# Performance work log

Measured on AMD Instinct MI355X. Metric: run time of the kernel, lower is better.

The kernel has to match this reference:

```python
import jax, jax.numpy as jnp
import numpy as np

N, E, L = 50000, 800000, 3
EPS = 1e-5


def mlp2(h, W1, b1, W2, b2):
    # Linear -> ReLU -> Linear
    return jax.nn.relu(h @ W1 + b1) @ W2 + b2


def setup_inputs() -> dict:
    key = jax.random.key(0)
    ks = jax.random.split(key, 20)
    s = 0.1  # weight scale to keep activations well-conditioned
    return {
        "x": jax.random.normal(ks[0], (N, 128), jnp.float32),
        "edge_attr": jax.random.normal(ks[1], (E, 64), jnp.float32),
        "edge_index": jax.random.randint(ks[2], (2, E), 0, N, dtype=jnp.int32),
        "Wn1": jax.random.normal(ks[3], (L, 128, 256), jnp.float32) * s,
        "bn1": jnp.zeros((L, 256), jnp.float32),
        "Wn2": jax.random.normal(ks[4], (L, 256, 128), jnp.float32) * s,
        "bn2": jnp.zeros((L, 128), jnp.float32),
        "We1": jax.random.normal(ks[5], (L, 64, 128), jnp.float32) * s,
        "be1": jnp.zeros((L, 128), jnp.float32),
        "We2": jax.random.normal(ks[6], (L, 128, 64), jnp.float32) * s,
        "be2": jnp.zeros((L, 64), jnp.float32),
        "Wm1": jax.random.normal(ks[7], (L, 320, 128), jnp.float32) * s,
        "bm1": jnp.zeros((L, 128), jnp.float32),
        "Wm2": jax.random.normal(ks[8], (L, 128, 128), jnp.float32) * s,
        "bm2": jnp.zeros((L, 128), jnp.float32),
        "lnw": jnp.ones((L, 128), jnp.float32),
        "lnb": jnp.zeros((L, 128), jnp.float32),
        "Wf": jax.random.normal(ks[9], (128, 64), jnp.float32) * s,
        "bf": jnp.zeros((64,), jnp.float32),
    }


def reference(x, edge_attr, edge_index, Wn1, bn1, Wn2, bn2, We1, be1, We2, be2,
              Wm1, bm1, Wm2, bm2, lnw, lnb, Wf, bf):
    src, dst = edge_index[0], edge_index[1]  # x_j = x[src], x_i = x[dst] (PyG source_to_target)
    deg = jax.ops.segment_sum(jnp.ones((E,), x.dtype), dst, num_segments=N)
    denom = jnp.maximum(deg, 1.0)[:, None]  # scatter-mean with clamp for isolated nodes
    for l in range(L):
        # mlp_node is the same function for x_i and x_j -> apply once per node, then gather
        xn = mlp2(x, Wn1[l], bn1[l], Wn2[l], bn2[l])        # [N, 128]
        e = mlp2(edge_attr, We1[l], be1[l], We2[l], be2[l])  # [E, 64]
        m = jnp.concatenate([xn[dst], xn[src], e], axis=-1)  # [E, 320] = [x_i, x_j, edge_attr]
        m = mlp2(m, Wm1[l], bm1[l], Wm2[l], bm2[l])          # [E, 128]
        agg = jax.ops.segment_sum(m, dst, num_segments=N) / denom  # mean aggregate [N, 128]
        mu = agg.mean(-1, keepdims=True)
        var = agg.var(-1, keepdims=True)
        h = (agg - mu) * jax.lax.rsqrt(var + EPS) * lnw[l] + lnb[l]  # LayerNorm
        x = jax.nn.relu(h)  # dropout p=0.0 -> identity
    return x @ Wf + bf  # jk='last' -> final linear on last layer output
```

## Files before the change

### kernel.cpp

```cpp
#include <hip/hip_runtime.h>
#include <stdint.h>

#define NN 50000
#define NE 800000
#define NB 196

typedef float f32x4 __attribute__((ext_vector_type(4)));
typedef short bf16x8 __attribute__((ext_vector_type(8)));

__device__ __forceinline__ unsigned short f2bf(float f) {
  union { float f; unsigned u; } v; v.f = f;
  unsigned r = v.u + 0x7fffu + ((v.u >> 16) & 1u);
  return (unsigned short)(r >> 16);
}
__device__ __forceinline__ float bf2f(unsigned short h) {
  union { unsigned u; float f; } v; v.u = ((unsigned)h) << 16;
  return v.f;
}
__device__ __forceinline__ float ldf(const void* p, size_t i, int m32) {
  return m32 ? ((const float*)p)[i] : bf2f(((const unsigned short*)p)[i]);
}

__global__ void detect_kernel(const void* lnw, int* flag) {
  if (threadIdx.x == 0 && blockIdx.x == 0)
    *flag = (((const unsigned short*)lnw)[0] == 0x3F80) ? 0 : 1;
}

#define oWn1 0
#define oWn2 98304
#define oWm1 196608
#define oWe1 319488
#define oWe2 344064
#define oWm2 368640
#define oWf  417792
#define NWTOT 425984
#define obn1 0
#define obn2 768
#define obe1 1152
#define obe2 1536
#define obm1 1728
#define obm2 2112
#define olnw 2496
#define olnb 2880
#define obf  3264
#define NBTOT 3328

__global__ __launch_bounds__(256) void conv_w(
    const void* Wn1, const void* Wn2, const void* Wm1, const void* We1,
    const void* We2, const void* Wm2, const void* Wf,
    const int* __restrict__ flg, unsigned short* __restrict__ cW)
{
  const int m32 = *flg;
  int i = blockIdx.x * 256 + threadIdx.x;
  if (i >= NWTOT) return;
  const void* src; size_t j;
  if      (i < oWn2) { src = Wn1; j = i - oWn1; }
  else if (i < oWm1) { src = Wn2; j = i - oWn2; }
  else if (i < oWe1) { src = Wm1; j = i - oWm1; }
  else if (i < oWe2) { src = We1; j = i - oWe1; }
  else if (i < oWm2) { src = We2; j = i - oWe2; }
  else if (i < oWf)  { src = Wm2; j = i - oWm2; }
  else               { src = Wf;  j = i - oWf;  }
  cW[i] = f2bf(ldf(src, j, m32));
}

__global__ __launch_bounds__(256) void conv_b(
    const void* bn1, const void* bn2, const void* be1, const void* be2,
    const void* bm1, const void* bm2, const void* lnw, const void* lnb,
    const void* bfv, const int* __restrict__ flg, float* __restrict__ cB)
{
  const int m32 = *flg;
  int i = blockIdx.x * 256 + threadIdx.x;
  if (i >= NBTOT) return;
  const void* src; size_t j;
  if      (i < obn2) { src = bn1; j = i - obn1; }
  else if (i < obe1) { src = bn2; j = i - obn2; }
  else if (i < obe2) { src = be1; j = i - obe1; }
  else if (i < obm1) { src = be2; j = i - obe2; }
  else if (i < obm2) { src = bm1; j = i - obm1; }
  else if (i < olnw) { src = bm2; j = i - obm2; }
  else if (i < olnb) { src = lnw; j = i - olnw; }
  else if (i < obf)  { src = lnb; j = i - olnb; }
  else               { src = bfv; j = i - obf;  }
  cB[i] = ldf(src, j, m32);
}

__global__ __launch_bounds__(256) void conv_x(const void* x, const int* flg,
                                              unsigned short* xc) {
  const int m32 = *flg;
  size_t i = (size_t)blockIdx.x * 256 + threadIdx.x;
  if (i < (size_t)NN * 128) xc[i] = f2bf(ldf(x, i, m32));
}

__global__ __launch_bounds__(256) void deg_int(const int* __restrict__ eidx,
                                               int* __restrict__ degi) {
  int i = blockIdx.x * 256 + threadIdx.x;
  if (i < NE) atomicAdd(degi + eidx[NE + i], 1);
}

__global__ __launch_bounds__(256) void scan1(const int* __restrict__ degi,
                                             int* __restrict__ base,
                                             int* __restrict__ bsum) {
  __shared__ int s[256];
  int t = threadIdx.x, i = blockIdx.x * 256 + t;
  int v = (i < NN) ? degi[i] : 0;
  s[t] = v; __syncthreads();
  for (int d = 1; d < 256; d <<= 1) {
    int u = (t >= d) ? s[t - d] : 0;
    __syncthreads();
    s[t] += u;
    __syncthreads();
  }
  if (i < NN) base[i] = s[t] - v;
  if (t == 255) bsum[blockIdx.x] = s[255];
}

__global__ void scan2(int* bsum) {
  __shared__ int s[256];
  int t = threadIdx.x;
  int v = (t < NB) ? bsum[t] : 0;
  s[t] = v; __syncthreads();
  for (int d = 1; d < 256; d <<= 1) {
    int u = (t >= d) ? s[t - d] : 0;
    __syncthreads();
    s[t] += u;
    __syncthreads();
  }
  if (t < NB) bsum[t] = s[t] - v;
}

__global__ __launch_bounds__(256) void scan3(int* base, const int* bsum) {
  int i = blockIdx.x * 256 + threadIdx.x;
  if (i < NN) base[i] += bsum[blockIdx.x];
}

__global__ __launch_bounds__(256) void scatter_sort(
    const int* __restrict__ eidx, const int* __restrict__ base,
    int* __restrict__ cursor, int* __restrict__ sE,
    int* __restrict__ sSrc, int* __restrict__ sDst) {
  int e = blockIdx.x * 256 + threadIdx.x;
  if (e < NE) {
    int s = eidx[e], d = eidx[NE + e];
    int r = atomicAdd(cursor + d, 1);
    int pos = base[d] + r;
    sE[pos] = e; sSrc[pos] = s; sDst[pos] = d;
  }
}

__global__ __launch_bounds__(256) void gather_ea(
    const void* __restrict__ ea, const int* __restrict__ sE,
    const int* __restrict__ flg, unsigned short* __restrict__ eaS) {
  const int m32 = *flg;
  int slot = blockIdx.x * 32 + (threadIdx.x >> 3);
  int j = threadIdx.x & 7;
  if (slot >= NE) return;
  int eid = sE[slot];
  unsigned short* dst = eaS + (size_t)slot * 64 + j * 8;
  if (m32) {
    const float* src = (const float*)ea + (size_t)eid * 64 + j * 8;
    f32x4 v0 = *(const f32x4*)src;
    f32x4 v1 = *(const f32x4*)(src + 4);
    alignas(16) unsigned short t[8];
    #pragma unroll
    for (int q = 0; q < 4; q++) { t[q] = f2bf(v0[q]); t[4 + q] = f2bf(v1[q]); }
    *(bf16x8*)dst = *(const bf16x8*)t;
  } else {
    const unsigned short* src = (const unsigned short*)ea + (size_t)eid * 64 + j * 8;
    *(bf16x8*)dst = *(const bf16x8*)src;
  }
}

__global__ __launch_bounds__(256) void prep_wc(
    const unsigned short* __restrict__ cW, const float* __restrict__ cB,
    float* __restrict__ Wc, float* __restrict__ bc2)
{
  int l = blockIdx.x;
  const unsigned short* We2l = cW + oWe2 + l * 8192;
  const unsigned short* Wm1c = cW + oWm1 + l * 40960 + 256 * 128;
  const float* be2l = cB + obe2 + l * 64;
  const float* bm1l = cB + obm1 + l * 128;
  float* out = Wc + l * 16384;
  for (int i = threadIdx.x; i < 16384; i += 256) {
    int k = i >> 7, n = i & 127;
    float s = 0.f;
    for (int u = 0; u < 64; u++)
      s += bf2f(We2l[k * 64 + u]) * bf2f(Wm1c[u * 128 + n]);
    out[i] = s;
  }
  if (threadIdx.x < 128) {
    int n = threadIdx.x;
    float s = bm1l[n];
    for (int u = 0; u < 64; u++)
      s += bf2f(be2l[u]) * bf2f(Wm1c[u * 128 + n]);
    bc2[l * 128 + n] = s;
  }
}

__global__ __launch_bounds__(256) void pack_frags(
    const unsigned short* __restrict__ cW, const float* __restrict__ Wcp,
    unsigned short* __restrict__ Wn1p, unsigned short* __restrict__ Wn2p,
    unsigned short* __restrict__ Wm1p, unsigned short* __restrict__ We1p,
    unsigned short* __restrict__ Wcpk, unsigned short* __restrict__ Wm2p)
{
  int l = blockIdx.x / 6, which = blockIdx.x % 6;
  int K, N, total;
  const unsigned short* src = nullptr;
  const float* srcf = nullptr;
  unsigned short* dst;
  if (which == 0)      { K = 128; N = 256; src = cW + oWn1 + (size_t)l * 32768; dst = Wn1p + (size_t)l * 32768; }
  else if (which == 1) { K = 256; N = 128; src = cW + oWn2 + (size_t)l * 32768; dst = Wn2p + (size_t)l * 32768; }
  else if (which == 2) { K = 128; N = 256; src = cW + oWm1 + (size_t)l * 40960; dst = Wm1p + (size_t)l * 32768; }
  else if (which == 3) { K = 64;  N = 128; src = cW + oWe1 + (size_t)l * 8192;  dst = We1p + (size_t)l * 8192; }
  else if (which == 4) { K = 128; N = 128; srcf = Wcp + (size_t)l * 16384;      dst = Wcpk + (size_t)l * 16384; }
  else                 { K = 128; N = 128; src = cW + oWm2 + (size_t)l * 16384; dst = Wm2p + (size_t)l * 16384; }
  int KB = K >> 5;
  total = K * N;
  for (int o = threadIdx.x; o < total; o += 256) {
    int j = o & 7, lane = (o >> 3) & 63, q = o >> 9;
    int kb = q % KB, c = q / KB;
    int k = kb * 32 + (lane >> 4) * 8 + j;
    int n = c * 16 + (lane & 15);
    unsigned short v;
    if (which == 2) {
      v = (n < 128) ? src[k * 128 + n] : src[(128 + k) * 128 + (n - 128)];
    } else if (which == 4) {
      v = f2bf(srcf[k * 128 + n]);
    } else {
      v = src[k * N + n];
    }
    dst[o] = v;
  }
}

__global__ __launch_bounds__(256) void node_p_mfma(
    const unsigned short* __restrict__ xin,
    const unsigned short* __restrict__ Wn1p, const unsigned short* __restrict__ Wn2p,
    const unsigned short* __restrict__ Wm1p, const float* __restrict__ cB,
    unsigned short* __restrict__ P, int l)
{
  __shared__ __align__(16) short HS[4][16 * 256];
  const int tid = threadIdx.x;
  const int wid = tid >> 6, lane = tid & 63, rl = lane & 15, cg = lane >> 4;
  const int n0 = blockIdx.x * 64;
  short* Hw = &HS[wid][0];
  const int swr = (rl & 7) << 3;

  int nA = n0 + wid * 16 + rl;
  int nAc = (nA < NN) ? nA : (NN - 1);

  bf16x8 ax[4];
  {
    const unsigned short* xr = xin + (size_t)nAc * 128;
    #pragma unroll
    for (int kb = 0; kb < 4; kb++)
      ax[kb] = *(const bf16x8*)&xr[kb * 32 + cg * 8];
  }

  {
    const unsigned short* Wb = Wn1p + (size_t)l * 32768;
    const float* b1 = cB + obn1 + l * 256;
    #pragma unroll
    for (int c = 0; c < 16; c++) {
      f32x4 acc = {0.f, 0.f, 0.f, 0.f};
      #pragma unroll
      for (int kb = 0; kb < 4; kb++) {
        bf16x8 b = *(const bf16x8*)&Wb[(size_t)(c * 4 + kb) * 512 + lane * 8];
        acc = __builtin_amdgcn_mfma_f32_16x16x32_bf16(ax[kb], b, acc, 0, 0, 0);
      }
      int col = c * 16 + rl;
      float bb = b1[col];
      #pragma unroll
      for (int r = 0; r < 4; r++) {
        int row = cg * 4 + r;
        Hw[row * 256 + (col ^ ((row & 7) << 3))] =
            (short)f2bf(fmaxf(acc[r] + bb, 0.f));
      }
    }
  }

  {
    bf16x8 ah[8];
    #pragma unroll
    for (int kb = 0; kb < 8; kb++)
      ah[kb] = *(const bf16x8*)&Hw[rl * 256 + ((kb * 32 + cg * 8) ^ swr)];
    const unsigned short* Wb = Wn2p + (size_t)l * 32768;
    const float* b2 = cB + obn2 + l * 128;
    #pragma unroll
    for (int c = 0; c < 8; c++) {
      f32x4 acc = {0.f, 0.f, 0.f, 0.f};
      #pragma unroll
      for (int kb = 0; kb < 8; kb++) {
        bf16x8 b = *(const bf16x8*)&Wb[(size_t)(c * 8 + kb) * 512 + lane * 8];
        acc = __builtin_amdgcn_mfma_f32_16x16x32_bf16(ah[kb], b, acc, 0, 0, 0);
      }
      int col = c * 16 + rl;
      float bb = b2[col];
      #pragma unroll
      for (int r = 0; r < 4; r++) {
        int row = cg * 4 + r;
        Hw[row * 128 + (col ^ ((row & 7) << 3))] = (short)f2bf(acc[r] + bb);
      }
    }
  }

  {
    bf16x8 an[4];
    #pragma unroll
    for (int kb = 0; kb < 4; kb++)
      an[kb] = *(const bf16x8*)&Hw[rl * 128 + ((kb * 32 + cg * 8) ^ swr)];
    const unsigned short* Wb = Wm1p + (size_t)l * 32768;
    #pragma unroll
    for (int c = 0; c < 16; c++) {
      f32x4 acc = {0.f, 0.f, 0.f, 0.f};
      #pragma unroll
      for (int kb = 0; kb < 4; kb++) {
        bf16x8 b = *(const bf16x8*)&Wb[(size_t)(c * 4 + kb) * 512 + lane * 8];
        acc = __builtin_amdgcn_mfma_f32_16x16x32_bf16(an[kb], b, acc, 0, 0, 0);
      }
      int col = c * 16 + rl;
      #pragma unroll
      for (int r = 0; r < 4; r++) {
        int row = cg * 4 + r;
        Hw[row * 256 + (col ^ ((row & 7) << 3))] = (short)f2bf(acc[r]);
      }
    }
  }
  {
    int row = lane >> 2;
    int ch = (lane & 3) * 64;
    int n = n0 + wid * 16 + row;
    if (n < NN) {
      int sw = (row & 7) << 3;
      unsigned short* dst = P + (size_t)n * 256 + ch;
      #pragma unroll
      for (int g = 0; g < 8; g++) {
        bf16x8 v = *(const bf16x8*)&Hw[row * 256 + ((ch + g * 8) ^ sw)];
        *(bf16x8*)(dst + g * 8) = v;
      }
    }
  }
}

__global__ __launch_bounds__(256, 8) void edge_fold_v5(
    const unsigned short* __restrict__ eaS,
    const int* __restrict__ sSrc, const int* __restrict__ sDst,
    const int* __restrict__ baseg, const int* __restrict__ degg,
    const unsigned short* __restrict__ We1p, const unsigned short* __restrict__ Wcpk,
    const float* __restrict__ cB, const float* __restrict__ bc2,
    const unsigned short* __restrict__ P, float* __restrict__ agg, int l)
{
  __shared__ __align__(16) short hS[64 * 136];
  __shared__ int dstS[64], srcS[64];
  const int tid = threadIdx.x;
  const int wid = tid >> 6, lane = tid & 63, rl = lane & 15, cg = lane >> 4;
  const int e0 = blockIdx.x * 64;
  short* Rw = hS + wid * 2048;
  const int swr = (rl & 7) << 3;
  const int brow = wid * 16 + rl;

  if (cg == 0) {
    dstS[brow] = sDst[e0 + brow];
    srcS[brow] = sSrc[e0 + brow];
  }

  const unsigned short* er = eaS + (size_t)(e0 + brow) * 64;
  bf16x8 a0 = *(const bf16x8*)&er[cg * 8];
  bf16x8 a1 = *(const bf16x8*)&er[32 + cg * 8];

  {
    const unsigned short* Wb = We1p + (size_t)l * 8192;
    const float* be1l = cB + obe1 + l * 128;
    #pragma unroll
    for (int c = 0; c < 8; c++) {
      bf16x8 b0 = *(const bf16x8*)&Wb[(c * 2 + 0) * 512 + lane * 8];
      bf16x8 b1 = *(const bf16x8*)&Wb[(c * 2 + 1) * 512 + lane * 8];
      f32x4 acc = {0.f, 0.f, 0.f, 0.f};
      acc = __builtin_amdgcn_mfma_f32_16x16x32_bf16(a0, b0, acc, 0, 0, 0);
      acc = __builtin_amdgcn_mfma_f32_16x16x32_bf16(a1, b1, acc, 0, 0, 0);
      int col = c * 16 + rl;
      float b = be1l[col];
      #pragma unroll
      for (int r = 0; r < 4; r++) {
        int row = cg * 4 + r;
        Rw[row * 128 + (col ^ ((row & 7) << 3))] =
            (short)f2bf(fmaxf(acc[r] + b, 0.f));
      }
    }
  }

  f32x4 acc2[8];
  {
    bf16x8 ra[4];
    #pragma unroll
    for (int kb = 0; kb < 4; kb++)
      ra[kb] = *(const bf16x8*)&Rw[rl * 128 + ((kb * 32 + cg * 8) ^ swr)];
    const unsigned short* Wb = Wcpk + (size_t)l * 16384;
    #pragma unroll
    for (int c = 0; c < 8; c++) {
      f32x4 acc = {0.f, 0.f, 0.f, 0.f};
      #pragma unroll
      for (int kb = 0; kb < 4; kb++) {
        bf16x8 b = *(const bf16x8*)&Wb[(c * 4 + kb) * 512 + lane * 8];
        acc = __builtin_amdgcn_mfma_f32_16x16x32_bf16(ra[kb], b, acc, 0, 0, 0);
      }
      acc2[c] = acc;
    }
  }

  __syncthreads();

  {
    const float* bc2l = bc2 + l * 128;
    #pragma unroll
    for (int c = 0; c < 8; c++) {
      int col = c * 16 + rl;
      float bv = bc2l[col];
      #pragma unroll
      for (int r = 0; r < 4; r++) {
        int row = wid * 16 + cg * 4 + r;
        hS[row * 136 + (col ^ ((row & 7) << 3))] =
            (short)f2bf(acc2[c][r] + bv);
      }
    }
  }
  __syncthreads();

  {
    int row = tid & 63;
    int ch = (tid >> 6) * 32;
    int di = dstS[row], si = srcS[row];
    int sw = (row & 7) << 3;
    const unsigned short* Pd = P + (size_t)di * 256 + ch;
    const unsigned short* Ps = P + (size_t)si * 256 + 128 + ch;
    #pragma unroll
    for (int g = 0; g < 4; g++) {
      bf16x8 pd = *(const bf16x8*)(Pd + g * 8);
      bf16x8 ps = *(const bf16x8*)(Ps + g * 8);
      short* hp = &hS[row * 136 + ((ch + g * 8) ^ sw)];
      bf16x8 hv = *(const bf16x8*)hp;
      alignas(16) unsigned short o[8];
      #pragma unroll
      for (int j = 0; j < 8; j++) {
        float h = bf2f((unsigned short)hv[j]) + bf2f((unsigned short)pd[j]) +
                  bf2f((unsigned short)ps[j]);
        o[j] = f2bf(fmaxf(h, 0.f));
      }
      *(bf16x8*)hp = *(const bf16x8*)o;
    }
  }
  __syncthreads();

  if (tid < 128) {
    const int col = tid;
    float run = 0.f;
    int cur = dstS[0];
    for (int i = 0; i < 64; i++) {
      int d = dstS[i];
      if (d != cur) {
        int b0 = baseg[cur], dg = degg[cur];
        if (b0 >= e0 && b0 + dg <= e0 + 64)
          agg[(size_t)cur * 128 + col] = run;
        else
          atomicAdd(agg + (size_t)cur * 128 + col, run);
        run = 0.f; cur = d;
      }
      run += bf2f((unsigned short)hS[i * 136 + (col ^ ((i & 7) << 3))]);
    }
    int b0 = baseg[cur], dg = degg[cur];
    if (b0 >= e0 && b0 + dg <= e0 + 64)
      agg[(size_t)cur * 128 + col] = run;
    else
      atomicAdd(agg + (size_t)cur * 128 + col, run);
  }
}

__global__ __launch_bounds__(256, 8) void agg_ln_mfma(
    const float* __restrict__ aggH, const int* __restrict__ degi,
    const unsigned short* __restrict__ Wm2p, const float* __restrict__ cB,
    unsigned short* __restrict__ xnext, int l)
{
  __shared__ __align__(16) short OS[4][16 * 136];
  const int tid = threadIdx.x;
  const int wid = tid >> 6, lane = tid & 63, rl = lane & 15, cg = lane >> 4;
  const int n0 = blockIdx.x * 64;
  short* Ow = &OS[wid][0];

  int nA = n0 + wid * 16 + rl;
  int nAc = (nA < NN) ? nA : (NN - 1);
  int dA = degi[nAc];
  float degf = (float)dA;
  float invd = 1.f / (float)(dA > 0 ? dA : 1);

  bf16x8 af[4];
  {
    const float* ar = aggH + (size_t)nAc * 128;
    #pragma unroll
    for (int kb = 0; kb < 4; kb++) {
      f32x4 v0 = *(const f32x4*)&ar[kb * 32 + cg * 8];
      f32x4 v1 = *(const f32x4*)&ar[kb * 32 + cg * 8 + 4];
      alignas(16) unsigned short t[8];
      #pragma unroll
      for (int q = 0; q < 4; q++) {
        t[q] = f2bf(v0[q] * invd);
        t[4 + q] = f2bf(v1[q] * invd);
      }
      af[kb] = *(const bf16x8*)t;
    }
  }

  f32x4 acc[8];
  {
    const unsigned short* Wb = Wm2p + (size_t)l * 16384;
    #pragma unroll
    for (int c = 0; c < 8; c++) {
      f32x4 a = {0.f, 0.f, 0.f, 0.f};
      #pragma unroll
      for (int kb = 0; kb < 4; kb++) {
        bf16x8 b = *(const bf16x8*)&Wb[(c * 4 + kb) * 512 + lane * 8];
        a = __builtin_amdgcn_mfma_f32_16x16x32_bf16(af[kb], b, a, 0, 0, 0);
      }
      acc[c] = a;
    }
  }

  const float* bm2p = cB + obm2 + l * 128;
  const float* lnwp = cB + olnw + l * 128;
  const float* lnbp = cB + olnb + l * 128;
  #pragma unroll
  for (int r = 0; r < 4; r++) {
    int row = cg * 4 + r;
    float dg = __shfl(degf, row, 64);
    float bmask = (dg > 0.f) ? 1.f : 0.f;
    float v[8];
    float s = 0.f, q = 0.f;
    #pragma unroll
    for (int c = 0; c < 8; c++) {
      float x = acc[c][r] + bmask * bm2p[c * 16 + rl];
      v[c] = x; s += x; q += x * x;
    }
    #pragma unroll
    for (int m = 1; m < 16; m <<= 1) {
      s += __shfl_xor(s, m, 64);
      q += __shfl_xor(q, m, 64);
    }
    float mu = s * (1.f / 128.f);
    float var = fmaxf(q * (1.f / 128.f) - mu * mu, 0.f);
    float rs = rsqrtf(var + 1e-5f);
    #pragma unroll
    for (int c = 0; c < 8; c++) {
      int col = c * 16 + rl;
      float y = fmaxf((v[c] - mu) * rs * lnwp[col] + lnbp[col], 0.f);
      Ow[row * 136 + (col ^ ((row & 7) << 3))] = (short)f2bf(y);
    }
  }
  {
    int row = lane >> 2;
    int ch = (lane & 3) * 32;
    int n = n0 + wid * 16 + row;
    if (n < NN) {
      int sw = (row & 7) << 3;
      unsigned short* dst = xnext + (size_t)n * 128 + ch;
      #pragma unroll
      for (int g = 0; g < 4; g++) {
        bf16x8 v = *(const bf16x8*)&Ow[row * 136 + ((ch + g * 8) ^ sw)];
        *(bf16x8*)(dst + g * 8) = v;
      }
    }
  }
}

__global__ __launch_bounds__(256) void final_k(
    const unsigned short* __restrict__ xc, const unsigned short* __restrict__ cW,
    const float* __restrict__ cB, const int* __restrict__ flg,
    void* __restrict__ out)
{
  const int m32 = *flg;
  const int tid = threadIdx.x;
  const int t = tid & 63;
  const int nd = blockIdx.x * 4 + (tid >> 6);
  float acc = cB[obf + t];
  const unsigned short* xr = xc + (size_t)nd * 128;
  const unsigned short* W = cW + oWf + t;
  for (int k = 0; k < 128; k++)
    acc += bf2f(xr[k]) * bf2f(W[(size_t)k * 64]);
  if (m32) ((float*)out)[(size_t)nd * 64 + t] = acc;
  else ((unsigned short*)out)[(size_t)nd * 64 + t] = f2bf(acc);
}

extern "C" void kernel_launch(void* const* d_in, const int* in_sizes, int n_in,
                              void* d_out, int out_size, void* d_ws, size_t ws_size,
                              hipStream_t stream) {
  (void)in_sizes; (void)n_in; (void)out_size; (void)ws_size;
  const void* x    = d_in[0];
  const void* ea   = d_in[1];
  const int*  eidx = (const int*)d_in[2];
  const void* Wn1  = d_in[3];
  const void* bn1  = d_in[4];
  const void* Wn2  = d_in[5];
  const void* bn2  = d_in[6];
  const void* We1  = d_in[7];
  const void* be1  = d_in[8];
  const void* We2  = d_in[9];
  const void* be2  = d_in[10];
  const void* Wm1  = d_in[11];
  const void* bm1  = d_in[12];
  const void* Wm2  = d_in[13];
  const void* bm2  = d_in[14];
  const void* lnw  = d_in[15];
  const void* lnb  = d_in[16];
  const void* Wf   = d_in[17];
  const void* bfv  = d_in[18];

  char* ws = (char*)d_ws;
  size_t off = 0;
  auto alloc = [&](size_t bytes) {
    size_t o = off;
    off += (bytes + 255) & ~(size_t)255;
    return o;
  };
  int*            flag = (int*)(ws + alloc(4));
  unsigned short* xcur = (unsigned short*)(ws + alloc((size_t)NN * 128 * 2));
  unsigned short* Pb   = (unsigned short*)(ws + alloc((size_t)NN * 256 * 2));
  float*          aggH = (float*)(ws + alloc((size_t)NN * 128 * 4));
  unsigned short* cW   = (unsigned short*)(ws + alloc((size_t)NWTOT * 2));
  float*          cB   = (float*)(ws + alloc((size_t)NBTOT * 4));
  float*          Wcp  = (float*)(ws + alloc(3 * 16384 * 4));
  float*          bc2w = (float*)(ws + alloc(3 * 128 * 4));
  unsigned short* We1p = (unsigned short*)(ws + alloc(3 * 8192 * 2));
  unsigned short* Wcpk = (unsigned short*)(ws + alloc(3 * 16384 * 2));
  unsigned short* Wn1p = (unsigned short*)(ws + alloc(3 * 32768 * 2));
  unsigned short* Wn2p = (unsigned short*)(ws + alloc(3 * 32768 * 2));
  unsigned short* Wm1p = (unsigned short*)(ws + alloc(3 * 32768 * 2));
  unsigned short* Wm2p = (unsigned short*)(ws + alloc(3 * 16384 * 2));
  int*            degi = (int*)(ws + alloc((size_t)NN * 4));
  int*            baseb= (int*)(ws + alloc((size_t)NN * 4));
  int*            bsum = (int*)(ws + alloc(256 * 4));
  int*            curs = (int*)(ws + alloc((size_t)NN * 4));
  int*            sE   = (int*)(ws + alloc((size_t)NE * 4));
  int*            sSrc = (int*)(ws + alloc((size_t)NE * 4));
  int*            sDst = (int*)(ws + alloc((size_t)NE * 4));
  unsigned short* eaS  = (unsigned short*)(ws + alloc((size_t)NE * 64 * 2));

  detect_kernel<<<1, 64, 0, stream>>>(lnw, flag);
  conv_w<<<(NWTOT + 255) / 256, 256, 0, stream>>>(Wn1, Wn2, Wm1, We1, We2, Wm2,
                                                  Wf, flag, cW);
  conv_b<<<(NBTOT + 255) / 256, 256, 0, stream>>>(bn1, bn2, be1, be2, bm1, bm2,
                                                  lnw, lnb, bfv, flag, cB);
  conv_x<<<(NN * 128 + 255) / 256, 256, 0, stream>>>(x, flag, xcur);

  hipMemsetAsync(degi, 0, (size_t)NN * 4, stream);
  deg_int<<<(NE + 255) / 256, 256, 0, stream>>>(eidx, degi);
  scan1<<<NB, 256, 0, stream>>>(degi, baseb, bsum);
  scan2<<<1, 256, 0, stream>>>(bsum);
  scan3<<<NB, 256, 0, stream>>>(baseb, bsum);
  hipMemsetAsync(curs, 0, (size_t)NN * 4, stream);
  scatter_sort<<<(NE + 255) / 256, 256, 0, stream>>>(eidx, baseb, curs, sE,
                                                     sSrc, sDst);
  gather_ea<<<NE / 32, 256, 0, stream>>>(ea, sE, flag, eaS);

  prep_wc<<<3, 256, 0, stream>>>(cW, cB, Wcp, bc2w);
  pack_frags<<<18, 256, 0, stream>>>(cW, Wcp, Wn1p, Wn2p, Wm1p, We1p, Wcpk,
                                     Wm2p);

  for (int l = 0; l < 3; l++) {
    node_p_mfma<<<(NN + 63) / 64, 256, 0, stream>>>(xcur, Wn1p, Wn2p, Wm1p,
                                                    cB, Pb, l);
    hipMemsetAsync(aggH, 0, (size_t)NN * 128 * 4, stream);
    edge_fold_v5<<<NE / 64, 256, 0, stream>>>(eaS, sSrc, sDst, baseb, degi,
                                              We1p, Wcpk, cB, bc2w, Pb,
                                              aggH, l);
    agg_ln_mfma<<<(NN + 63) / 64, 256, 0, stream>>>(aggH, degi, Wm2p, cB,
                                                    xcur, l);
  }
  final_k<<<NN / 4, 256, 0, stream>>>(xcur, cW, cB, flag, d_out);
}
```

Measured before the change: 1.525 ms.

## Prefetch P gathers before barrier, split segment reduction across all threads, drop swizzle

The edge kernel now loads the src/dst indices straight into registers and issues the gathers of projected node features early, before the barrier that precedes the hS bias write. This lets gather latency overlap the MFMA epilogue. The segmented reduction now uses all 256 threads, with each half handling 32 edges, rather than only 128 threads walking 64. The XOR swizzle on the padded 136-stride LDS rows is removed in both edge_fold and agg_ln. Holding the prefetched data raises register pressure, so launch bounds go from 8 to 6 waves, and splitting the reduction produces more atomics at the half boundary.

```diff
diff --git a/kernel.cpp b/kernel.cpp
--- a/kernel.cpp
+++ b/kernel.cpp
@@ -341,7 +341,7 @@
   }
 }
 
-__global__ __launch_bounds__(256, 8) void edge_fold_v5(
+__global__ __launch_bounds__(256, 6) void edge_fold_v6(
     const unsigned short* __restrict__ eaS,
     const int* __restrict__ sSrc, const int* __restrict__ sDst,
     const int* __restrict__ baseg, const int* __restrict__ degg,
@@ -350,7 +350,7 @@
     const unsigned short* __restrict__ P, float* __restrict__ agg, int l)
 {
   __shared__ __align__(16) short hS[64 * 136];
-  __shared__ int dstS[64], srcS[64];
+  __shared__ int dstS[64];
   const int tid = threadIdx.x;
   const int wid = tid >> 6, lane = tid & 63, rl = lane & 15, cg = lane >> 4;
   const int e0 = blockIdx.x * 64;
@@ -358,10 +358,12 @@
   const int swr = (rl & 7) << 3;
   const int brow = wid * 16 + rl;
 
-  if (cg == 0) {
-    dstS[brow] = sDst[e0 + brow];
-    srcS[brow] = sSrc[e0 + brow];
-  }
+  if (cg == 0) dstS[brow] = sDst[e0 + brow];
+
+  const int row2 = tid & 63;
+  const int ch2 = (tid >> 6) * 32;
+  const int di2 = sDst[e0 + row2];
+  const int si2 = sSrc[e0 + row2];
 
   const unsigned short* er = eaS + (size_t)(e0 + brow) * 64;
   bf16x8 a0 = *(const bf16x8*)&er[cg * 8];
@@ -407,6 +409,17 @@
     }
   }
 
+  bf16x8 pd[4], ps[4];
+  {
+    const unsigned short* Pd = P + (size_t)di2 * 256 + ch2;
+    const unsigned short* Ps = P + (size_t)si2 * 256 + 128 + ch2;
+    #pragma unroll
+    for (int g = 0; g < 4; g++) {
+      pd[g] = *(const bf16x8*)(Pd + g * 8);
+      ps[g] = *(const bf16x8*)(Ps + g * 8);
+    }
+  }
+
   __syncthreads();
 
   {
@@ -418,31 +431,22 @@
       #pragma unroll
       for (int r = 0; r < 4; r++) {
         int row = wid * 16 + cg * 4 + r;
-        hS[row * 136 + (col ^ ((row & 7) << 3))] =
-            (short)f2bf(acc2[c][r] + bv);
+        hS[row * 136 + col] = (short)f2bf(acc2[c][r] + bv);
       }
     }
   }
   __syncthreads();
 
   {
-    int row = tid & 63;
-    int ch = (tid >> 6) * 32;
-    int di = dstS[row], si = srcS[row];
-    int sw = (row & 7) << 3;
-    const unsigned short* Pd = P + (size_t)di * 256 + ch;
-    const unsigned short* Ps = P + (size_t)si * 256 + 128 + ch;
     #pragma unroll
     for (int g = 0; g < 4; g++) {
-      bf16x8 pd = *(const bf16x8*)(Pd + g * 8);
-      bf16x8 ps = *(const bf16x8*)(Ps + g * 8);
-      short* hp = &hS[row * 136 + ((ch + g * 8) ^ sw)];
+      short* hp = &hS[row2 * 136 + ch2 + g * 8];
       bf16x8 hv = *(const bf16x8*)hp;
       alignas(16) unsigned short o[8];
       #pragma unroll
       for (int j = 0; j < 8; j++) {
-        float h = bf2f((unsigned short)hv[j]) + bf2f((unsigned short)pd[j]) +
-                  bf2f((unsigned short)ps[j]);
+        float h = bf2f((unsigned short)hv[j]) + bf2f((unsigned short)pd[g][j]) +
+                  bf2f((unsigned short)ps[g][j]);
         o[j] = f2bf(fmaxf(h, 0.f));
       }
       *(bf16x8*)hp = *(const bf16x8*)o;
@@ -450,24 +454,26 @@
   }
   __syncthreads();
 
-  if (tid < 128) {
-    const int col = tid;
+  {
+    const int col = tid & 127;
+    const int half = tid >> 7;
+    const int lo = half * 32, hi = lo + 32;
     float run = 0.f;
-    int cur = dstS[0];
-    for (int i = 0; i < 64; i++) {
+    int cur = dstS[lo];
+    for (int i = lo; i < hi; i++) {
       int d = dstS[i];
       if (d != cur) {
         int b0 = baseg[cur], dg = degg[cur];
-        if (b0 >= e0 && b0 + dg <= e0 + 64)
+        if (b0 >= e0 + lo && b0 + dg <= e0 + hi)
           agg[(size_t)cur * 128 + col] = run;
         else
           atomicAdd(agg + (size_t)cur * 128 + col, run);
         run = 0.f; cur = d;
       }
-      run += bf2f((unsigned short)hS[i * 136 + (col ^ ((i & 7) << 3))]);
+      run += bf2f((unsigned short)hS[i * 136 + col]);
     }
     int b0 = baseg[cur], dg = degg[cur];
-    if (b0 >= e0 && b0 + dg <= e0 + 64)
+    if (b0 >= e0 + lo && b0 + dg <= e0 + hi)
       agg[(size_t)cur * 128 + col] = run;
     else
       atomicAdd(agg + (size_t)cur * 128 + col, run);
@@ -550,7 +556,7 @@
     for (int c = 0; c < 8; c++) {
       int col = c * 16 + rl;
       float y = fmaxf((v[c] - mu) * rs * lnwp[col] + lnbp[col], 0.f);
-      Ow[row * 136 + (col ^ ((row & 7) << 3))] = (short)f2bf(y);
+      Ow[row * 136 + col] = (short)f2bf(y);
     }
   }
   {
@@ -558,11 +564,10 @@
     int ch = (lane & 3) * 32;
     int n = n0 + wid * 16 + row;
     if (n < NN) {
-      int sw = (row & 7) << 3;
       unsigned short* dst = xnext + (size_t)n * 128 + ch;
       #pragma unroll
       for (int g = 0; g < 4; g++) {
-        bf16x8 v = *(const bf16x8*)&Ow[row * 136 + ((ch + g * 8) ^ sw)];
+        bf16x8 v = *(const bf16x8*)&Ow[row * 136 + ch + g * 8];
         *(bf16x8*)(dst + g * 8) = v;
       }
     }
@@ -666,7 +671,7 @@
     node_p_mfma<<<(NN + 63) / 64, 256, 0, stream>>>(xcur, Wn1p, Wn2p, Wm1p,
                                                     cB, Pb, l);
     hipMemsetAsync(aggH, 0, (size_t)NN * 128 * 4, stream);
-    edge_fold_v5<<<NE / 64, 256, 0, stream>>>(eaS, sSrc, sDst, baseb, degi,
+    edge_fold_v6<<<NE / 64, 256, 0, stream>>>(eaS, sSrc, sDst, baseb, degi,
                                               We1p, Wcpk, cB, bc2w, Pb,
                                               aggH, l);
     agg_ln_mfma<<<(NN + 63) / 64, 256, 0, stream>>>(aggH, degi, Wm2p, cB,
```

Result: faster. 1.472 ms (-3.5%).
